# Optimization experiments

Measured on AMD Instinct MI355X. Metric: run time of the kernel, lower is better.

Reference implementation:

```python
import jax, jax.numpy as jnp
import numpy as np

# model_grid_shape (flipped ensemble grid, all equal here); E = 8 experts
GRID = (2, 2, 2)
E = GRID[0] * GRID[1] * GRID[2]
N = 524288   # query points
H = 64       # sub-model MLP hidden width


def setup_inputs() -> dict:
    key = jax.random.key(0)
    ks = jax.random.split(key, 4)
    # query coordinates in [-1, 1]^3
    x = jax.random.uniform(ks[0], (N, 3), jnp.float32, -1.0, 1.0)
    # per-expert spatial extents: axis-aligned cells tiling [-1,1]^3, in the
    # same flat order as the routing index i0 + i1*g0 + i2*g0*g1
    i = np.arange(E)
    cell = np.stack([i % GRID[0], (i // GRID[0]) % GRID[1],
                     i // (GRID[0] * GRID[1])], axis=-1).astype(np.float32)
    g = np.array(GRID, np.float32)
    extents_min = jnp.asarray(-1.0 + 2.0 * cell / g)          # [E, 3]
    extents_max = jnp.asarray(-1.0 + 2.0 * (cell + 1.0) / g)  # [E, 3]
    # per-expert SRN MLP parameters: 3 -> H -> H -> 1
    W1 = jax.random.normal(ks[1], (E, 3, H), jnp.float32) / np.sqrt(3.0)
    b1 = jnp.zeros((E, H), jnp.float32)
    W2 = jax.random.normal(ks[2], (E, H, H), jnp.float32) / np.sqrt(float(H))
    b2 = jnp.zeros((E, H), jnp.float32)
    W3 = jax.random.normal(ks[3], (E, H, 1), jnp.float32) / np.sqrt(float(H))
    b3 = jnp.zeros((E, 1), jnp.float32)
    return {"x": x, "extents_min": extents_min, "extents_max": extents_max,
            "W1": W1, "b1": b1, "W2": W2, "b2": b2, "W3": W3, "b3": b3}


def reference(x, extents_min, extents_max, W1, b1, W2, b2, W3, b3):
    # --- routing: flat expert index per point (matches torch forward) ---
    u = jnp.clip((x + 1.0) * 0.5, 0.0, 0.99)
    gvec = jnp.asarray(GRID, x.dtype)
    gi = (u * gvec).astype(jnp.int32)                       # [N, 3]
    idx = gi[:, 0] + gi[:, 1] * GRID[0] + gi[:, 2] * (GRID[0] * GRID[1])

    # --- dispatch/combine: scan over experts, masked scatter into y ---
    def body(y, args):
        i, emin, emax, w1, bb1, w2, bb2, w3, bb3 = args
        # normalize point into expert-local [-1, 1]^3
        xn = -1.0 + 2.0 * ((x - emin) / (emax - emin))      # [N, 3]
        h = jax.nn.relu(xn @ w1 + bb1)                      # [N, H]
        h = jax.nn.relu(h @ w2 + bb2)                       # [N, H]
        o = h @ w3 + bb3                                    # [N, 1]
        mask = (idx == i)[:, None]
        return jnp.where(mask, o, y), None

    y0 = jnp.zeros((x.shape[0], 1), x.dtype)
    y, _ = jax.lax.scan(
        body, y0,
        (jnp.arange(E), extents_min, extents_max, W1, b1, W2, b2, W3, b3))
    return y
```

## Files before the change

### kernel.cpp

```cpp
#include <hip/hip_runtime.h>

typedef __bf16 bf16x8 __attribute__((ext_vector_type(8)));
typedef __bf16 bf16x2 __attribute__((ext_vector_type(2)));
typedef float f32x4 __attribute__((ext_vector_type(4)));
typedef float f32x2 __attribute__((ext_vector_type(2)));

#define N_PTS 524288
#define SBLK 256
#define PTS_PER_SBLK 2048
#define CAP 73728
#define POISON 0xAAAAAAAAu

__device__ __forceinline__ unsigned short f2bf(float f) {
    unsigned u = __float_as_uint(f);
    u += 0x7FFFu + ((u >> 16) & 1u);
    return (unsigned short)(u >> 16);
}

__device__ __forceinline__ unsigned decode(unsigned c) {
    return (c >= POISON) ? (c - POISON) : c;
}

__device__ __forceinline__ int route(float x0, float x1, float x2) {
    int g0 = (int)(fminf(fmaxf((x0 + 1.0f) * 0.5f, 0.0f), 0.99f) * 2.0f);
    int g1 = (int)(fminf(fmaxf((x1 + 1.0f) * 0.5f, 0.0f), 0.99f) * 2.0f);
    int g2 = (int)(fminf(fmaxf((x2 + 1.0f) * 0.5f, 0.0f), 0.99f) * 2.0f);
    return g0 + 2*g1 + 4*g2;
}

#define OFF_CNT  0u
#define OFF_XG   1024u

extern "C" __global__ void __launch_bounds__(256) k3_scatter(
        const float* __restrict__ x, int* __restrict__ cursor,
        float4* __restrict__ xg) {
    __shared__ int lh[8];
    __shared__ int startS[8];
    int t = threadIdx.x;
    if (t < 8) lh[t] = 0;
    __syncthreads();
    int base = blockIdx.x * PTS_PER_SBLK;
    float c0[8], c1[8], c2[8];
    unsigned epack = 0;
    #pragma unroll
    for (int i = 0; i < 8; ++i) {
        int p = base + i * 256 + t;
        c0[i] = x[3*p]; c1[i] = x[3*p+1]; c2[i] = x[3*p+2];
        int e = route(c0[i], c1[i], c2[i]);
        epack |= (unsigned)e << (3*i);
        atomicAdd(&lh[e], 1);
    }
    __syncthreads();
    if (t < 8) {
        unsigned claim = (unsigned)atomicAdd(&cursor[t], lh[t]);
        startS[t] = (int)decode(claim);
        lh[t] = 0;
    }
    __syncthreads();
    #pragma unroll
    for (int i = 0; i < 8; ++i) {
        int e = (epack >> (3*i)) & 7;
        int r = atomicAdd(&lh[e], 1);
        float4 v;
        v.x = c0[i]; v.y = c1[i]; v.z = c2[i];
        v.w = __uint_as_float((unsigned)(base + i * 256 + t));
        xg[e*CAP + startS[e] + r] = v;
    }
}

extern "C" __global__ void __launch_bounds__(256, 3) k4_mlp(
        const float4* __restrict__ xg, const int* __restrict__ cursor,
        const float* __restrict__ emin, const float* __restrict__ emax,
        const float* __restrict__ W1, const float* __restrict__ b1,
        const float* __restrict__ W2, const float* __restrict__ b2,
        const float* __restrict__ W3, const float* __restrict__ b3,
        float* __restrict__ y) {
    int e = blockIdx.y;
    int cnt = (int)decode((unsigned)cursor[e]);
    int tileStart = blockIdx.x * 256;
    if (tileStart >= cnt) return;
    int base = e * CAP;

    int t = threadIdx.x;
    int lane = t & 63, wave = t >> 6;
    int m16 = lane & 15;
    int g  = lane >> 4;
    int g8 = g * 8;

    __shared__ __align__(16) unsigned short h1s[256][72];
    __shared__ __align__(16) unsigned short w2t[64][72];
    __shared__ float4 w1s[64];
    __shared__ float  b2s[64], w3s[64];

    if (t < 64) {
        int n = t;
        float d0 = emax[e*3+0] - emin[e*3+0];
        float d1 = emax[e*3+1] - emin[e*3+1];
        float d2 = emax[e*3+2] - emin[e*3+2];
        float a0 = 2.0f/d0, a1 = 2.0f/d1, a2 = 2.0f/d2;
        float cc0 = -1.0f - 2.0f*emin[e*3+0]/d0;
        float cc1 = -1.0f - 2.0f*emin[e*3+1]/d1;
        float cc2 = -1.0f - 2.0f*emin[e*3+2]/d2;
        float w0 = W1[(e*3+0)*64 + n];
        float w1 = W1[(e*3+1)*64 + n];
        float w2 = W1[(e*3+2)*64 + n];
        float4 w;
        w.x = a0*w0; w.y = a1*w1; w.z = a2*w2;
        w.w = cc0*w0 + cc1*w1 + cc2*w2 + b1[e*64 + n];
        w1s[n] = w;
    } else if (t < 128) {
        b2s[t - 64]  = b2[e*64 + (t - 64)];
    } else if (t < 192) {
        w3s[t - 128] = W3[e*64 + (t - 128)];
    }
    #pragma unroll
    for (int i = 0; i < 16; ++i) {
        int idx = i * 256 + t;
        int k = idx >> 6, n = idx & 63;
        w2t[n][k] = f2bf(W2[(e*64 + k)*64 + n]);
    }

    int valid = (tileStart + t) < cnt;
    float px = 0.f, py = 0.f, pz = 0.f;
    unsigned pidx = 0;
    if (valid) {
        float4 v = xg[base + tileStart + t];
        px = v.x; py = v.y; pz = v.z; pidx = __float_as_uint(v.w);
    }
    __syncthreads();

    #pragma unroll
    for (int jb = 0; jb < 8; ++jb) {
        bf16x8 hv;
        #pragma unroll
        for (int j2 = 0; j2 < 8; j2 += 2) {
            float4 wa = w1s[jb*8 + j2];
            float4 wb = w1s[jb*8 + j2 + 1];
            float ha = fmaf(px, wa.x, fmaf(py, wa.y, fmaf(pz, wa.z, wa.w)));
            float hb = fmaf(px, wb.x, fmaf(py, wb.y, fmaf(pz, wb.z, wb.w)));
            f32x2 hp;
            hp[0] = fmaxf(ha, 0.0f);
            hp[1] = fmaxf(hb, 0.0f);
            bf16x2 bp = __builtin_convertvector(hp, bf16x2);
            hv[j2] = bp[0]; hv[j2+1] = bp[1];
        }
        *(bf16x8*)(&h1s[t][jb*8]) = hv;
    }
    __syncthreads();

    bf16x8 A[4][2];
    #pragma unroll
    for (int mt = 0; mt < 4; ++mt)
        #pragma unroll
        for (int kt = 0; kt < 2; ++kt)
            A[mt][kt] = *(const bf16x8*)(&w2t[mt*16 + m16][kt*32 + g8]);

    f32x4 acc[4][4] = {};
    #pragma unroll
    for (int pt = 0; pt < 4; ++pt) {
        int row = wave*64 + pt*16 + m16;
        bf16x8 B0 = *(const bf16x8*)(&h1s[row][g8]);
        bf16x8 B1 = *(const bf16x8*)(&h1s[row][32 + g8]);
        #pragma unroll
        for (int mt = 0; mt < 4; ++mt) {
            acc[mt][pt] = __builtin_amdgcn_mfma_f32_16x16x32_bf16(A[mt][0], B0, acc[mt][pt], 0, 0, 0);
            acc[mt][pt] = __builtin_amdgcn_mfma_f32_16x16x32_bf16(A[mt][1], B1, acc[mt][pt], 0, 0, 0);
        }
    }

    float bb3 = b3[e];
    #pragma unroll
    for (int pt = 0; pt < 4; ++pt) {
        float s = 0.0f;
        #pragma unroll
        for (int mt = 0; mt < 4; ++mt) {
            #pragma unroll
            for (int r = 0; r < 4; ++r) {
                int f = mt*16 + g*4 + r;
                float h2 = fmaxf(acc[mt][pt][r] + b2s[f], 0.0f);
                s = fmaf(h2, w3s[f], s);
            }
        }
        s += __shfl_xor(s, 16, 64);
        s += __shfl_xor(s, 32, 64);
        unsigned oi = (unsigned)__shfl((int)pidx, pt*16 + m16, 64);
        int row = wave*64 + pt*16 + m16;
        if (lane < 16 && (tileStart + row) < cnt) {
            y[oi] = s + bb3;
        }
    }
}

extern "C" void kernel_launch(void* const* d_in, const int* in_sizes, int n_in,
                              void* d_out, int out_size, void* d_ws, size_t ws_size,
                              hipStream_t stream) {
    const float* x    = (const float*)d_in[0];
    const float* emin = (const float*)d_in[1];
    const float* emax = (const float*)d_in[2];
    const float* W1   = (const float*)d_in[3];
    const float* b1   = (const float*)d_in[4];
    const float* W2   = (const float*)d_in[5];
    const float* b2   = (const float*)d_in[6];
    const float* W3   = (const float*)d_in[7];
    const float* b3   = (const float*)d_in[8];
    float* y = (float*)d_out;

    char* ws = (char*)d_ws;
    int*  cursor = (int*)(ws + OFF_CNT);
    float4* xg   = (float4*)(ws + OFF_XG);

    k3_scatter<<<SBLK, 256, 0, stream>>>(x, cursor, xg);
    k4_mlp<<<dim3(288, 8), 256, 0, stream>>>(xg, cursor, emin, emax,
                                             W1, b1, W2, b2, W3, b3, y);
}
```

Baseline: 96.43 us.

## Quantize routed points to packed 64-bit records and vectorize scatter loads

The scatter kernel now applies each expert's local normalization itself and quantizes the three coordinates to 15 bits each, packing them with the point index into one 64-bit word instead of a 16-byte float4. This halves the intermediate gather buffer traffic, and the MLP kernel decodes coordinates with a single fma per axis using the raw W1/b1. The scatter kernel also reads x as contiguous float4 loads covering 4 points per thread, with twice as many blocks. Quantizing inputs to 15 bits adds approximation error on top of the existing bf16 hidden layer, which may affect tolerance.

After: 97.87 us. Within noise of the previous version (+1.5%).

```diff
diff --git a/kernel.cpp b/kernel.cpp
--- a/kernel.cpp
+++ b/kernel.cpp
@@ -6,10 +6,12 @@
 typedef float f32x2 __attribute__((ext_vector_type(2)));
 
 #define N_PTS 524288
-#define SBLK 256
-#define PTS_PER_SBLK 2048
+#define SBLK 512
+#define PTS_PER_SBLK 1024
 #define CAP 73728
 #define POISON 0xAAAAAAAAu
+#define QSCALE 16383.5f
+#define QINV   6.1038882e-05f
 
 __device__ __forceinline__ unsigned short f2bf(float f) {
     unsigned u = __float_as_uint(f);
@@ -28,27 +30,43 @@
     return g0 + 2*g1 + 4*g2;
 }
 
+__device__ __forceinline__ unsigned quant(float a, float c, float xv) {
+    float xn = fmaf(a, xv, c);
+    float q = fminf(fmaxf((xn + 1.0f) * QSCALE, 0.0f), 32767.0f);
+    return __float2uint_rn(q);
+}
+
 #define OFF_CNT  0u
 #define OFF_XG   1024u
 
 extern "C" __global__ void __launch_bounds__(256) k3_scatter(
-        const float* __restrict__ x, int* __restrict__ cursor,
-        float4* __restrict__ xg) {
+        const float* __restrict__ x,
+        const float* __restrict__ emin, const float* __restrict__ emax,
+        int* __restrict__ cursor, unsigned long long* __restrict__ xg8) {
     __shared__ int lh[8];
     __shared__ int startS[8];
+    __shared__ float aeS[8][3], ceS[8][3];
     int t = threadIdx.x;
     if (t < 8) lh[t] = 0;
-    __syncthreads();
-    int base = blockIdx.x * PTS_PER_SBLK;
-    float c0[8], c1[8], c2[8];
-    unsigned epack = 0;
-    #pragma unroll
-    for (int i = 0; i < 8; ++i) {
-        int p = base + i * 256 + t;
-        c0[i] = x[3*p]; c1[i] = x[3*p+1]; c2[i] = x[3*p+2];
-        int e = route(c0[i], c1[i], c2[i]);
-        epack |= (unsigned)e << (3*i);
-        atomicAdd(&lh[e], 1);
+    if (t < 24) {
+        int e = t / 3, ax = t % 3;
+        float mn = emin[e*3 + ax];
+        float d  = emax[e*3 + ax] - mn;
+        aeS[e][ax] = 2.0f / d;
+        ceS[e][ax] = -1.0f - 2.0f * mn / d;
+    }
+    __syncthreads();
+    int p0 = blockIdx.x * PTS_PER_SBLK + 4 * t;
+    const float4* xv = (const float4*)(x + 3 * p0);
+    float4 v0 = xv[0], v1 = xv[1], v2 = xv[2];
+    float c0[4] = {v0.x, v0.w, v1.z, v2.y};
+    float c1[4] = {v0.y, v1.x, v1.w, v2.z};
+    float c2[4] = {v0.z, v1.y, v2.x, v2.w};
+    int ev[4];
+    #pragma unroll
+    for (int i = 0; i < 4; ++i) {
+        ev[i] = route(c0[i], c1[i], c2[i]);
+        atomicAdd(&lh[ev[i]], 1);
     }
     __syncthreads();
     if (t < 8) {
@@ -58,19 +76,22 @@
     }
     __syncthreads();
     #pragma unroll
-    for (int i = 0; i < 8; ++i) {
-        int e = (epack >> (3*i)) & 7;
+    for (int i = 0; i < 4; ++i) {
+        int e = ev[i];
         int r = atomicAdd(&lh[e], 1);
-        float4 v;
-        v.x = c0[i]; v.y = c1[i]; v.z = c2[i];
-        v.w = __uint_as_float((unsigned)(base + i * 256 + t));
-        xg[e*CAP + startS[e] + r] = v;
+        unsigned q0 = quant(aeS[e][0], ceS[e][0], c0[i]);
+        unsigned q1 = quant(aeS[e][1], ceS[e][1], c1[i]);
+        unsigned q2 = quant(aeS[e][2], ceS[e][2], c2[i]);
+        unsigned long long pk = (unsigned long long)q0
+                              | ((unsigned long long)q1 << 15)
+                              | ((unsigned long long)q2 << 30)
+                              | ((unsigned long long)(unsigned)(p0 + i) << 45);
+        xg8[e*CAP + startS[e] + r] = pk;
     }
 }
 
 extern "C" __global__ void __launch_bounds__(256, 3) k4_mlp(
-        const float4* __restrict__ xg, const int* __restrict__ cursor,
-        const float* __restrict__ emin, const float* __restrict__ emax,
+        const unsigned long long* __restrict__ xg8, const int* __restrict__ cursor,
         const float* __restrict__ W1, const float* __restrict__ b1,
         const float* __restrict__ W2, const float* __restrict__ b2,
         const float* __restrict__ W3, const float* __restrict__ b3,
@@ -94,19 +115,11 @@
 
     if (t < 64) {
         int n = t;
-        float d0 = emax[e*3+0] - emin[e*3+0];
-        float d1 = emax[e*3+1] - emin[e*3+1];
-        float d2 = emax[e*3+2] - emin[e*3+2];
-        float a0 = 2.0f/d0, a1 = 2.0f/d1, a2 = 2.0f/d2;
-        float cc0 = -1.0f - 2.0f*emin[e*3+0]/d0;
-        float cc1 = -1.0f - 2.0f*emin[e*3+1]/d1;
-        float cc2 = -1.0f - 2.0f*emin[e*3+2]/d2;
-        float w0 = W1[(e*3+0)*64 + n];
-        float w1 = W1[(e*3+1)*64 + n];
-        float w2 = W1[(e*3+2)*64 + n];
         float4 w;
-        w.x = a0*w0; w.y = a1*w1; w.z = a2*w2;
-        w.w = cc0*w0 + cc1*w1 + cc2*w2 + b1[e*64 + n];
+        w.x = W1[(e*3+0)*64 + n];
+        w.y = W1[(e*3+1)*64 + n];
+        w.z = W1[(e*3+2)*64 + n];
+        w.w = b1[e*64 + n];
         w1s[n] = w;
     } else if (t < 128) {
         b2s[t - 64]  = b2[e*64 + (t - 64)];
@@ -124,8 +137,11 @@
     float px = 0.f, py = 0.f, pz = 0.f;
     unsigned pidx = 0;
     if (valid) {
-        float4 v = xg[base + tileStart + t];
-        px = v.x; py = v.y; pz = v.z; pidx = __float_as_uint(v.w);
+        unsigned long long v = xg8[base + tileStart + t];
+        px = fmaf((float)(unsigned)( v        & 0x7FFFu), QINV, -1.0f);
+        py = fmaf((float)(unsigned)((v >> 15) & 0x7FFFu), QINV, -1.0f);
+        pz = fmaf((float)(unsigned)((v >> 30) & 0x7FFFu), QINV, -1.0f);
+        pidx = (unsigned)(v >> 45);
     }
     __syncthreads();
 
@@ -206,10 +222,9 @@
     float* y = (float*)d_out;
 
     char* ws = (char*)d_ws;
-    int*  cursor = (int*)(ws + OFF_CNT);
-    float4* xg   = (float4*)(ws + OFF_XG);
-
-    k3_scatter<<<SBLK, 256, 0, stream>>>(x, cursor, xg);
-    k4_mlp<<<dim3(288, 8), 256, 0, stream>>>(xg, cursor, emin, emax,
-                                             W1, b1, W2, b2, W3, b3, y);
-}
+    int* cursor = (int*)(ws + OFF_CNT);
+    unsigned long long* xg8 = (unsigned long long*)(ws + OFF_XG);
+
+    k3_scatter<<<SBLK, 256, 0, stream>>>(x, emin, emax, cursor, xg8);
+    k4_mlp<<<dim3(288, 8), 256, 0, stream>>>(xg8, cursor, W1, b1, W2, b2, W3, b3, y);
+}
```
